# Kernel tuning notes

Hardware: AMD Instinct MI355X
Metric: run time of the kernel (lower is better)

## Reference

```python
import jax, jax.numpy as jnp
import numpy as np

B, N, D, E, H, K = 2, 2048, 1024, 8, 2048, 2


def setup_inputs() -> dict:
    key = jax.random.key(0)
    ks = jax.random.split(key, 5)
    s = 0.02  # init scale
    return {
        "x": jax.random.normal(ks[0], (B, N, D), dtype=jnp.float32),
        "w_gate": jax.random.normal(ks[1], (D, E), dtype=jnp.float32) * s,
        "b_gate": jnp.zeros((E,), dtype=jnp.float32),
        "w1": jax.random.normal(ks[2], (E, D, H), dtype=jnp.float32) * s,
        "b1": jnp.zeros((E, H), dtype=jnp.float32),
        "w2": jax.random.normal(ks[3], (E, H, D), dtype=jnp.float32) * s,
        "b2": jnp.zeros((E, D), dtype=jnp.float32),
    }


def reference(x, w_gate, b_gate, w1, b1, w2, b2):
    b, n, d = x.shape
    T = b * n
    xf = x.reshape(T, d)                                   # (T, D)
    # --- top-k routing ---
    logits = xf @ w_gate + b_gate                          # (T, E)
    topk_logits, topk_idx = jax.lax.top_k(logits, K)       # (T, K)
    topk_gates = jax.nn.softmax(topk_logits, axis=-1)      # softmax over selected experts
    entropy = -(topk_gates * jnp.log(jnp.clip(topk_gates, 1e-8, None))).sum(-1).mean()
    # scatter top-k gates into full (T, E) gate matrix (zeros for unselected)
    gates = jnp.zeros_like(logits).at[jnp.arange(T)[:, None], topk_idx].add(topk_gates)
    # --- expert MLPs (dense over experts; gates zero out unselected) ---
    h = jax.nn.relu(jnp.einsum('td,edh->eth', xf, w1) + b1[:, None, :])  # (E, T, H)
    y = jnp.einsum('eth,ehd->etd', h, w2) + b2[:, None, :]               # (E, T, D)
    out = jnp.einsum('etd,te->td', y, gates).reshape(b, n, d)
    return out, entropy
```

## Files before the change

kernel.cpp:

```cpp
#include <hip/hip_runtime.h>

#define T_TOK 4096
#define D_DIM 1024
#define E_EXP 8
#define H_DIM 2048
#define CAP   9216
#define TILES_M 72

typedef __attribute__((ext_vector_type(8))) short bf16x8;
typedef __attribute__((ext_vector_type(4))) float f32x4;

__device__ inline unsigned short f2bf(float f) {
    unsigned int u = __float_as_uint(f);
    unsigned int r = (u + 0x7fffu + ((u >> 16) & 1u)) >> 16;
    return (unsigned short)r;
}

#define GLD_LDS16(g, l)                                                        \
    __builtin_amdgcn_global_load_lds(                                          \
        (const __attribute__((address_space(1))) void*)(g),                    \
        (__attribute__((address_space(3))) void*)(l), 16, 0, 0)

__global__ void cvt_kernel(const float* __restrict__ src,
                           unsigned short* __restrict__ dst, int n4) {
    int i = blockIdx.x * blockDim.x + threadIdx.x;
    int stride = gridDim.x * blockDim.x;
    for (; i < n4; i += stride) {
        float4 v = ((const float4*)src)[i];
        ushort4 o;
        o.x = f2bf(v.x); o.y = f2bf(v.y); o.z = f2bf(v.z); o.w = f2bf(v.w);
        ((ushort4*)dst)[i] = o;
    }
}

__global__ __launch_bounds__(256) void tcvt_kernel(const float* __restrict__ src,
                                                   unsigned short* __restrict__ dst,
                                                   int R, int C) {
    __shared__ float tile[64][65];
    size_t eo = (size_t)blockIdx.z * R * C;
    src += eo; dst += eo;
    int tx = threadIdx.x & 15, ty = threadIdx.x >> 4;
    int c0 = blockIdx.x * 64, r0 = blockIdx.y * 64;
    #pragma unroll
    for (int i = 0; i < 4; i++) {
        int row = ty + i * 16;
        float4 v = *(const float4*)&src[(size_t)(r0 + row) * C + c0 + tx * 4];
        tile[row][tx * 4 + 0] = v.x;
        tile[row][tx * 4 + 1] = v.y;
        tile[row][tx * 4 + 2] = v.z;
        tile[row][tx * 4 + 3] = v.w;
    }
    __syncthreads();
    #pragma unroll
    for (int i = 0; i < 4; i++) {
        int cc = ty + i * 16;
        int rr = tx * 4;
        ushort4 o;
        o.x = f2bf(tile[rr + 0][cc]);
        o.y = f2bf(tile[rr + 1][cc]);
        o.z = f2bf(tile[rr + 2][cc]);
        o.w = f2bf(tile[rr + 3][cc]);
        *(ushort4*)&dst[(size_t)(c0 + cc) * R + r0 + rr] = o;
    }
}

__global__ __launch_bounds__(256) void gating_kernel(
    const float* __restrict__ xf, const float* __restrict__ wg,
    const float* __restrict__ bg, int* __restrict__ tk_e,
    float* __restrict__ tk_g, float* __restrict__ ent_part)
{
    __shared__ float ents[4];
    int wave = threadIdx.x >> 6, lane = threadIdx.x & 63;
    int t = blockIdx.x * 4 + wave;
    const float* xr = xf + (size_t)t * D_DIM;
    float acc[8] = {0.f,0.f,0.f,0.f,0.f,0.f,0.f,0.f};
    for (int i = 0; i < 16; i++) {
        int d = lane + i * 64;
        float xv = xr[d];
        const float4* wr = (const float4*)(wg + (size_t)d * 8);
        float4 w0 = wr[0], w1 = wr[1];
        acc[0] += xv * w0.x; acc[1] += xv * w0.y; acc[2] += xv * w0.z; acc[3] += xv * w0.w;
        acc[4] += xv * w1.x; acc[5] += xv * w1.y; acc[6] += xv * w1.z; acc[7] += xv * w1.w;
    }
    #pragma unroll
    for (int s = 1; s < 64; s <<= 1) {
        #pragma unroll
        for (int e = 0; e < 8; e++) acc[e] += __shfl_xor(acc[e], s, 64);
    }
    if (lane == 0) {
        float l[8];
        #pragma unroll
        for (int e = 0; e < 8; e++) l[e] = acc[e] + bg[e];
        int i0 = 0;
        #pragma unroll
        for (int e = 1; e < 8; e++) if (l[e] > l[i0]) i0 = e;
        int i1 = (i0 == 0) ? 1 : 0;
        #pragma unroll
        for (int e = 0; e < 8; e++) if (e != i0 && l[e] > l[i1]) i1 = e;
        float z  = expf(l[i1] - l[i0]);
        float p0 = 1.0f / (1.0f + z);
        float p1 = z / (1.0f + z);
        float ent = -(p0 * logf(fmaxf(p0, 1e-8f)) + p1 * logf(fmaxf(p1, 1e-8f)));
        ents[wave] = ent;
        tk_e[t * 2 + 0] = i0; tk_g[t * 2 + 0] = p0;
        tk_e[t * 2 + 1] = i1; tk_g[t * 2 + 1] = p1;
    }
    __syncthreads();
    if (threadIdx.x == 0)
        ent_part[blockIdx.x] = ents[0] + ents[1] + ents[2] + ents[3];
}

__global__ __launch_bounds__(256) void ent_reduce_kernel(
    const float* __restrict__ ent_part, float* __restrict__ ent_out)
{
    __shared__ float ws_[4];
    int tid = threadIdx.x;
    float s = 0.f;
    for (int i = tid; i < T_TOK / 4; i += 256) s += ent_part[i];
    #pragma unroll
    for (int d = 1; d < 64; d <<= 1) s += __shfl_xor(s, d, 64);
    if ((tid & 63) == 0) ws_[tid >> 6] = s;
    __syncthreads();
    if (tid == 0)
        *ent_out = (ws_[0] + ws_[1] + ws_[2] + ws_[3]) * (1.0f / T_TOK);
}

__global__ __launch_bounds__(1024) void route_kernel(
    const int* __restrict__ tk_e, const float* __restrict__ tk_g,
    int* __restrict__ off, int* __restrict__ slot_token,
    float* __restrict__ slot_gate, int* __restrict__ slot_of)
{
    __shared__ int wt[16][8];
    __shared__ int wx[16][8];
    __shared__ int base[9];
    __shared__ int tot[8];

    int tid = threadIdx.x, wid = tid >> 6, lane = tid & 63;
    int i0 = tid * 8;
    int ev[8];
    *(int4*)&ev[0] = *(const int4*)&tk_e[i0];
    *(int4*)&ev[4] = *(const int4*)&tk_e[i0 + 4];

    unsigned own[4] = {0u, 0u, 0u, 0u};
    #pragma unroll
    for (int j = 0; j < 8; j++) {
        int e = ev[j];
        int reg = ((e < 4) ? 0 : 2) + (e & 1);
        own[reg] += 1u << (((e >> 1) & 1) * 16);
    }
    unsigned inc[4] = {own[0], own[1], own[2], own[3]};
    #pragma unroll
    for (int d = 1; d < 64; d <<= 1) {
        #pragma unroll
        for (int k = 0; k < 4; k++) {
            unsigned t = __shfl_up(inc[k], d, 64);
            if (lane >= d) inc[k] += t;
        }
    }
    if (lane == 63) {
        #pragma unroll
        for (int e = 0; e < 8; e++) {
            int reg = ((e < 4) ? 0 : 2) + (e & 1);
            wt[wid][e] = (inc[reg] >> (((e >> 1) & 1) * 16)) & 0xFFFF;
        }
    }
    __syncthreads();
    if (tid == 0) {
        int o = 0;
        for (int e = 0; e < 8; e++) {
            int run = 0;
            for (int w = 0; w < 16; w++) { wx[w][e] = run; run += wt[w][e]; }
            tot[e] = run;
            base[e] = o;
            off[e] = o;
            o += (run + 127) & ~127;
        }
        base[8] = o;
        off[8] = o;
    }
    __syncthreads();

    #pragma unroll
    for (int e = 0; e < 8; e++) {
        int p0 = base[e] + tot[e], p1 = base[e + 1];
        for (int i = p0 + tid; i < p1; i += 1024) slot_token[i] = -1;
    }

    unsigned run[4] = {0u, 0u, 0u, 0u};
    #pragma unroll
    for (int j = 0; j < 8; j++) {
        int e = ev[j];
        int reg = ((e < 4) ? 0 : 2) + (e & 1);
        int sh = ((e >> 1) & 1) * 16;
        int lx = (int)(((inc[reg] - own[reg]) >> sh) & 0xFFFF);
        int lr = (int)((run[reg] >> sh) & 0xFFFF);
        int slot = base[e] + wx[wid][e] + lx + lr;
        run[reg] += 1u << sh;
        int i = i0 + j;
        slot_token[slot] = i >> 1;
        slot_gate[slot] = tk_g[i];
        slot_of[i] = slot;
    }
}

__global__ __launch_bounds__(256) void gemm1_kernel(
    const unsigned short* __restrict__ xb, const unsigned short* __restrict__ w1t,
    const float* __restrict__ b1g, const int* __restrict__ off,
    const int* __restrict__ slot_token, unsigned short* __restrict__ Hb)
{
    __shared__ __align__(16) unsigned short As[128 * 32];
    __shared__ __align__(16) unsigned short Bs[128 * 32];

    int s0 = blockIdx.x * 128;
    if (s0 >= off[E_EXP]) return;
    int e = 0;
    while (s0 >= off[e + 1]) e++;
    int n0 = blockIdx.y * 128;

    int tid = threadIdx.x;
    int wave = tid >> 6, lane = tid & 63;
    int lrow = lane & 15, quad = lane >> 4;
    int srow = lane >> 2;
    int scol = (lane & 3) * 8;

    int r0 = 32 * wave + srow, r1 = r0 + 16;
    int t0 = slot_token[s0 + r0]; if (t0 < 0) t0 = 0;
    int t1 = slot_token[s0 + r1]; if (t1 < 0) t1 = 0;
    const unsigned short* a0 = xb + (size_t)t0 * D_DIM + scol;
    const unsigned short* a1 = xb + (size_t)t1 * D_DIM + scol;
    const unsigned short* wb = w1t + (size_t)e * H_DIM * D_DIM;
    const unsigned short* bp0 = wb + (size_t)(n0 + r0) * D_DIM + scol;
    const unsigned short* bp1 = wb + (size_t)(n0 + r1) * D_DIM + scol;

    unsigned short* lA0 = As + wave * 1024;
    unsigned short* lA1 = lA0 + 512;
    unsigned short* lB0 = Bs + wave * 1024;
    unsigned short* lB1 = lB0 + 512;

    f32x4 acc[4][4];
    #pragma unroll
    for (int mi = 0; mi < 4; mi++)
        #pragma unroll
        for (int ni = 0; ni < 4; ni++) acc[mi][ni] = (f32x4){0.f, 0.f, 0.f, 0.f};

    int wr = (wave >> 1) * 64, wc = (wave & 1) * 64;

    for (int k0 = 0; k0 < D_DIM; k0 += 32) {
        __syncthreads();
        GLD_LDS16(a0 + k0, lA0);
        GLD_LDS16(a1 + k0, lA1);
        GLD_LDS16(bp0 + k0, lB0);
        GLD_LDS16(bp1 + k0, lB1);
        __syncthreads();
        bf16x8 af[4], bfr[4];
        #pragma unroll
        for (int i = 0; i < 4; i++) {
            af[i]  = *(const bf16x8*)&As[(wr + i * 16 + lrow) * 32 + quad * 8];
            bfr[i] = *(const bf16x8*)&Bs[(wc + i * 16 + lrow) * 32 + quad * 8];
        }
        #pragma unroll
        for (int mi = 0; mi < 4; mi++)
            #pragma unroll
            for (int ni = 0; ni < 4; ni++)
                acc[mi][ni] = __builtin_amdgcn_mfma_f32_16x16x32_bf16(
                    af[mi], bfr[ni], acc[mi][ni], 0, 0, 0);
    }

    #pragma unroll
    for (int ni = 0; ni < 4; ni++) {
        int col = wc + ni * 16 + lrow;
        int h = n0 + col;
        float bv = b1g[e * H_DIM + h];
        #pragma unroll
        for (int mi = 0; mi < 4; mi++) {
            int mrow = wr + mi * 16 + quad * 4;
            #pragma unroll
            for (int r = 0; r < 4; r++) {
                float v = fmaxf(acc[mi][ni][r] + bv, 0.0f);
                Hb[(size_t)(s0 + mrow + r) * H_DIM + h] = f2bf(v);
            }
        }
    }
}

__global__ __launch_bounds__(256) void gemm2_kernel(
    const unsigned short* __restrict__ Hb, const unsigned short* __restrict__ w2t,
    const float* __restrict__ b2g, const int* __restrict__ off,
    unsigned short* __restrict__ Yb)
{
    __shared__ __align__(16) unsigned short As[128 * 32];
    __shared__ __align__(16) unsigned short Bs[128 * 32];

    int s0 = blockIdx.x * 128;
    if (s0 >= off[E_EXP]) return;
    int e = 0;
    while (s0 >= off[e + 1]) e++;
    int n0 = blockIdx.y * 128;

    int tid = threadIdx.x;
    int wave = tid >> 6, lane = tid & 63;
    int lrow = lane & 15, quad = lane >> 4;
    int srow = lane >> 2;
    int scol = (lane & 3) * 8;

    int r0 = 32 * wave + srow, r1 = r0 + 16;
    const unsigned short* a0 = Hb + (size_t)(s0 + r0) * H_DIM + scol;
    const unsigned short* a1 = Hb + (size_t)(s0 + r1) * H_DIM + scol;
    const unsigned short* wb = w2t + (size_t)e * D_DIM * H_DIM;
    const unsigned short* bp0 = wb + (size_t)(n0 + r0) * H_DIM + scol;
    const unsigned short* bp1 = wb + (size_t)(n0 + r1) * H_DIM + scol;

    unsigned short* lA0 = As + wave * 1024;
    unsigned short* lA1 = lA0 + 512;
    unsigned short* lB0 = Bs + wave * 1024;
    unsigned short* lB1 = lB0 + 512;

    f32x4 acc[4][4];
    #pragma unroll
    for (int mi = 0; mi < 4; mi++)
        #pragma unroll
        for (int ni = 0; ni < 4; ni++) acc[mi][ni] = (f32x4){0.f, 0.f, 0.f, 0.f};

    int wr = (wave >> 1) * 64, wc = (wave & 1) * 64;

    for (int k0 = 0; k0 < H_DIM; k0 += 32) {
        __syncthreads();
        GLD_LDS16(a0 + k0, lA0);
        GLD_LDS16(a1 + k0, lA1);
        GLD_LDS16(bp0 + k0, lB0);
        GLD_LDS16(bp1 + k0, lB1);
        __syncthreads();
        bf16x8 af[4], bfr[4];
        #pragma unroll
        for (int i = 0; i < 4; i++) {
            af[i]  = *(const bf16x8*)&As[(wr + i * 16 + lrow) * 32 + quad * 8];
            bfr[i] = *(const bf16x8*)&Bs[(wc + i * 16 + lrow) * 32 + quad * 8];
        }
        #pragma unroll
        for (int mi = 0; mi < 4; mi++)
            #pragma unroll
            for (int ni = 0; ni < 4; ni++)
                acc[mi][ni] = __builtin_amdgcn_mfma_f32_16x16x32_bf16(
                    af[mi], bfr[ni], acc[mi][ni], 0, 0, 0);
    }

    #pragma unroll
    for (int ni = 0; ni < 4; ni++) {
        int col = wc + ni * 16 + lrow;
        int d = n0 + col;
        float bv = b2g[e * D_DIM + d];
        #pragma unroll
        for (int mi = 0; mi < 4; mi++) {
            int mrow = wr + mi * 16 + quad * 4;
            #pragma unroll
            for (int r = 0; r < 4; r++) {
                Yb[(size_t)(s0 + mrow + r) * D_DIM + d] = f2bf(acc[mi][ni][r] + bv);
            }
        }
    }
}

__global__ __launch_bounds__(256) void combine_kernel(
    const unsigned short* __restrict__ Yb, const int* __restrict__ slot_of,
    const float* __restrict__ tk_g, float* __restrict__ out)
{
    int t = blockIdx.x * 2 + (threadIdx.x >> 7);
    int j = threadIdx.x & 127;
    int sA = slot_of[t * 2], sB = slot_of[t * 2 + 1];
    float gA = tk_g[t * 2], gB = tk_g[t * 2 + 1];
    uint4 va = *(const uint4*)(Yb + (size_t)sA * D_DIM + j * 8);
    uint4 vb = *(const uint4*)(Yb + (size_t)sB * D_DIM + j * 8);
    const unsigned int* pa = (const unsigned int*)&va;
    const unsigned int* pb = (const unsigned int*)&vb;
    float o[8];
    #pragma unroll
    for (int i = 0; i < 4; i++) {
        float a_lo = __uint_as_float(pa[i] << 16);
        float a_hi = __uint_as_float(pa[i] & 0xffff0000u);
        float b_lo = __uint_as_float(pb[i] << 16);
        float b_hi = __uint_as_float(pb[i] & 0xffff0000u);
        o[i * 2 + 0] = gA * a_lo + gB * b_lo;
        o[i * 2 + 1] = gA * a_hi + gB * b_hi;
    }
    float* op = out + (size_t)t * D_DIM + j * 8;
    ((float4*)op)[0] = make_float4(o[0], o[1], o[2], o[3]);
    ((float4*)op)[1] = make_float4(o[4], o[5], o[6], o[7]);
}

extern "C" void kernel_launch(void* const* d_in, const int* in_sizes, int n_in,
                              void* d_out, int out_size, void* d_ws, size_t ws_size,
                              hipStream_t stream)
{
    const float* xf = (const float*)d_in[0];
    const float* wg = (const float*)d_in[1];
    const float* bg = (const float*)d_in[2];
    const float* w1 = (const float*)d_in[3];
    const float* b1 = (const float*)d_in[4];
    const float* w2 = (const float*)d_in[5];
    const float* b2 = (const float*)d_in[6];
    float* out = (float*)d_out;

    char* p = (char*)d_ws;
    int* off    = (int*)p;
    int* tk_e   = off + 16;
    float* tk_g = (float*)(tk_e + T_TOK * 2);
    int* slot_token = (int*)(tk_g + T_TOK * 2);
    float* slot_gate = (float*)(slot_token + CAP);
    int* slot_of = (int*)(slot_gate + CAP);
    float* ent_part = (float*)(slot_of + T_TOK * 2);
    size_t ofs = ((size_t)((char*)(ent_part + T_TOK / 4) - p) + 255) & ~(size_t)255;
    unsigned short* xb  = (unsigned short*)(p + ofs); ofs += (size_t)T_TOK * D_DIM * 2;
    unsigned short* w1t = (unsigned short*)(p + ofs); ofs += (size_t)E_EXP * D_DIM * H_DIM * 2;
    unsigned short* w2t = (unsigned short*)(p + ofs); ofs += (size_t)E_EXP * H_DIM * D_DIM * 2;
    unsigned short* Hb  = (unsigned short*)(p + ofs); ofs += (size_t)CAP * H_DIM * 2;
    unsigned short* Yb  = w1t;

    cvt_kernel<<<1024, 256, 0, stream>>>(xf, xb, T_TOK * D_DIM / 4);
    tcvt_kernel<<<dim3(H_DIM / 64, D_DIM / 64, E_EXP), 256, 0, stream>>>(w1, w1t, D_DIM, H_DIM);
    tcvt_kernel<<<dim3(D_DIM / 64, H_DIM / 64, E_EXP), 256, 0, stream>>>(w2, w2t, H_DIM, D_DIM);

    gating_kernel<<<T_TOK / 4, 256, 0, stream>>>(xf, wg, bg, tk_e, tk_g, ent_part);
    ent_reduce_kernel<<<1, 256, 0, stream>>>(ent_part, out + (size_t)T_TOK * D_DIM);
    route_kernel<<<1, 1024, 0, stream>>>(tk_e, tk_g, off, slot_token, slot_gate, slot_of);
    gemm1_kernel<<<dim3(TILES_M, H_DIM / 128), 256, 0, stream>>>(xb, w1t, b1, off,
                                                                 slot_token, Hb);
    gemm2_kernel<<<dim3(TILES_M, D_DIM / 128), 256, 0, stream>>>(Hb, w2t, b2, off, Yb);
    combine_kernel<<<T_TOK / 2, 256, 0, stream>>>(Yb, slot_of, tk_g, out);
}
```

Baseline: 341.0 us.

## Fuse x conversion into gating, merge entropy reduce, swizzle LDS, vectorize GEMM stores

```diff
diff --git a/kernel.cpp b/kernel.cpp
--- a/kernel.cpp
+++ b/kernel.cpp
@@ -20,18 +20,6 @@
     __builtin_amdgcn_global_load_lds(                                          \
         (const __attribute__((address_space(1))) void*)(g),                    \
         (__attribute__((address_space(3))) void*)(l), 16, 0, 0)
-
-__global__ void cvt_kernel(const float* __restrict__ src,
-                           unsigned short* __restrict__ dst, int n4) {
-    int i = blockIdx.x * blockDim.x + threadIdx.x;
-    int stride = gridDim.x * blockDim.x;
-    for (; i < n4; i += stride) {
-        float4 v = ((const float4*)src)[i];
-        ushort4 o;
-        o.x = f2bf(v.x); o.y = f2bf(v.y); o.z = f2bf(v.z); o.w = f2bf(v.w);
-        ((ushort4*)dst)[i] = o;
-    }
-}
 
 __global__ __launch_bounds__(256) void tcvt_kernel(const float* __restrict__ src,
                                                    unsigned short* __restrict__ dst,
@@ -66,17 +54,20 @@
 
 __global__ __launch_bounds__(256) void gating_kernel(
     const float* __restrict__ xf, const float* __restrict__ wg,
-    const float* __restrict__ bg, int* __restrict__ tk_e,
-    float* __restrict__ tk_g, float* __restrict__ ent_part)
+    const float* __restrict__ bg, unsigned short* __restrict__ xb,
+    int* __restrict__ tk_e, float* __restrict__ tk_g,
+    float* __restrict__ ent_part)
 {
     __shared__ float ents[4];
     int wave = threadIdx.x >> 6, lane = threadIdx.x & 63;
     int t = blockIdx.x * 4 + wave;
     const float* xr = xf + (size_t)t * D_DIM;
+    unsigned short* xbr = xb + (size_t)t * D_DIM;
     float acc[8] = {0.f,0.f,0.f,0.f,0.f,0.f,0.f,0.f};
     for (int i = 0; i < 16; i++) {
         int d = lane + i * 64;
         float xv = xr[d];
+        xbr[d] = f2bf(xv);
         const float4* wr = (const float4*)(wg + (size_t)d * 8);
         float4 w0 = wr[0], w1 = wr[1];
         acc[0] += xv * w0.x; acc[1] += xv * w0.y; acc[2] += xv * w0.z; acc[3] += xv * w0.w;
@@ -110,36 +101,28 @@
         ent_part[blockIdx.x] = ents[0] + ents[1] + ents[2] + ents[3];
 }
 
-__global__ __launch_bounds__(256) void ent_reduce_kernel(
-    const float* __restrict__ ent_part, float* __restrict__ ent_out)
-{
-    __shared__ float ws_[4];
-    int tid = threadIdx.x;
-    float s = 0.f;
-    for (int i = tid; i < T_TOK / 4; i += 256) s += ent_part[i];
-    #pragma unroll
-    for (int d = 1; d < 64; d <<= 1) s += __shfl_xor(s, d, 64);
-    if ((tid & 63) == 0) ws_[tid >> 6] = s;
-    __syncthreads();
-    if (tid == 0)
-        *ent_out = (ws_[0] + ws_[1] + ws_[2] + ws_[3]) * (1.0f / T_TOK);
-}
-
 __global__ __launch_bounds__(1024) void route_kernel(
     const int* __restrict__ tk_e, const float* __restrict__ tk_g,
     int* __restrict__ off, int* __restrict__ slot_token,
-    float* __restrict__ slot_gate, int* __restrict__ slot_of)
+    float* __restrict__ slot_gate, int* __restrict__ slot_of,
+    const float* __restrict__ ent_part, float* __restrict__ ent_out)
 {
     __shared__ int wt[16][8];
     __shared__ int wx[16][8];
     __shared__ int base[9];
     __shared__ int tot[8];
+    __shared__ float es[16];
 
     int tid = threadIdx.x, wid = tid >> 6, lane = tid & 63;
     int i0 = tid * 8;
     int ev[8];
     *(int4*)&ev[0] = *(const int4*)&tk_e[i0];
     *(int4*)&ev[4] = *(const int4*)&tk_e[i0 + 4];
+
+    float s = ent_part[tid];
+    #pragma unroll
+    for (int d = 1; d < 64; d <<= 1) s += __shfl_xor(s, d, 64);
+    if (lane == 0) es[wid] = s;
 
     unsigned own[4] = {0u, 0u, 0u, 0u};
     #pragma unroll
@@ -177,6 +160,9 @@
         }
         base[8] = o;
         off[8] = o;
+        float se = 0.f;
+        for (int w = 0; w < 16; w++) se += es[w];
+        *ent_out = se * (1.0f / T_TOK);
     }
     __syncthreads();
 
@@ -221,21 +207,21 @@
     int wave = tid >> 6, lane = tid & 63;
     int lrow = lane & 15, quad = lane >> 4;
     int srow = lane >> 2;
-    int scol = (lane & 3) * 8;
-
-    int r0 = 32 * wave + srow, r1 = r0 + 16;
+    int scol = ((lane & 3) ^ ((srow >> 1) & 3)) * 8;
+
+    int r0 = 16 * wave + srow, r1 = r0 + 64;
     int t0 = slot_token[s0 + r0]; if (t0 < 0) t0 = 0;
     int t1 = slot_token[s0 + r1]; if (t1 < 0) t1 = 0;
+    const unsigned short* wb = w1t + (size_t)e * H_DIM * D_DIM;
     const unsigned short* a0 = xb + (size_t)t0 * D_DIM + scol;
     const unsigned short* a1 = xb + (size_t)t1 * D_DIM + scol;
-    const unsigned short* wb = w1t + (size_t)e * H_DIM * D_DIM;
     const unsigned short* bp0 = wb + (size_t)(n0 + r0) * D_DIM + scol;
     const unsigned short* bp1 = wb + (size_t)(n0 + r1) * D_DIM + scol;
 
-    unsigned short* lA0 = As + wave * 1024;
-    unsigned short* lA1 = lA0 + 512;
-    unsigned short* lB0 = Bs + wave * 1024;
-    unsigned short* lB1 = lB0 + 512;
+    unsigned short* lA0 = As + (16 * wave) * 32;
+    unsigned short* lA1 = As + (64 + 16 * wave) * 32;
+    unsigned short* lB0 = Bs + (16 * wave) * 32;
+    unsigned short* lB1 = Bs + (64 + 16 * wave) * 32;
 
     f32x4 acc[4][4];
     #pragma unroll
@@ -244,6 +230,7 @@
         for (int ni = 0; ni < 4; ni++) acc[mi][ni] = (f32x4){0.f, 0.f, 0.f, 0.f};
 
     int wr = (wave >> 1) * 64, wc = (wave & 1) * 64;
+    int g = (quad ^ ((lrow >> 1) & 3)) * 8;
 
     for (int k0 = 0; k0 < D_DIM; k0 += 32) {
         __syncthreads();
@@ -255,8 +242,8 @@
         bf16x8 af[4], bfr[4];
         #pragma unroll
         for (int i = 0; i < 4; i++) {
-            af[i]  = *(const bf16x8*)&As[(wr + i * 16 + lrow) * 32 + quad * 8];
-            bfr[i] = *(const bf16x8*)&Bs[(wc + i * 16 + lrow) * 32 + quad * 8];
+            af[i]  = *(const bf16x8*)&As[(wr + i * 16 + lrow) * 32 + g];
+            bfr[i] = *(const bf16x8*)&Bs[(wc + i * 16 + lrow) * 32 + g];
         }
         #pragma unroll
         for (int mi = 0; mi < 4; mi++)
@@ -266,20 +253,25 @@
                     af[mi], bfr[ni], acc[mi][ni], 0, 0, 0);
     }
 
-    #pragma unroll
-    for (int ni = 0; ni < 4; ni++) {
-        int col = wc + ni * 16 + lrow;
-        int h = n0 + col;
-        float bv = b1g[e * H_DIM + h];
-        #pragma unroll
-        for (int mi = 0; mi < 4; mi++) {
-            int mrow = wr + mi * 16 + quad * 4;
+    float bv[4];
+    #pragma unroll
+    for (int ni = 0; ni < 4; ni++) bv[ni] = b1g[e * H_DIM + n0 + wc + ni * 16 + lrow];
+    unsigned short* w = As + wave * 1024;
+    __syncthreads();
+    #pragma unroll
+    for (int mi = 0; mi < 4; mi++) {
+        #pragma unroll
+        for (int ni = 0; ni < 4; ni++)
             #pragma unroll
-            for (int r = 0; r < 4; r++) {
-                float v = fmaxf(acc[mi][ni][r] + bv, 0.0f);
-                Hb[(size_t)(s0 + mrow + r) * H_DIM + h] = f2bf(v);
-            }
-        }
+            for (int r = 0; r < 4; r++)
+                w[(quad * 4 + r) * 64 + ni * 16 + lrow] =
+                    f2bf(fmaxf(acc[mi][ni][r] + bv[ni], 0.0f));
+        int rd = lane >> 3, cc = (lane & 7) * 8;
+        bf16x8 v0 = *(const bf16x8*)&w[rd * 64 + cc];
+        bf16x8 v1 = *(const bf16x8*)&w[(8 + rd) * 64 + cc];
+        size_t rowg = (size_t)(s0 + wr + mi * 16 + rd) * H_DIM + n0 + wc + cc;
+        *(bf16x8*)&Hb[rowg] = v0;
+        *(bf16x8*)&Hb[rowg + 8 * H_DIM] = v1;
     }
 }
 
@@ -301,19 +293,19 @@
     int wave = tid >> 6, lane = tid & 63;
     int lrow = lane & 15, quad = lane >> 4;
     int srow = lane >> 2;
-    int scol = (lane & 3) * 8;
-
-    int r0 = 32 * wave + srow, r1 = r0 + 16;
+    int scol = ((lane & 3) ^ ((srow >> 1) & 3)) * 8;
+
+    int r0 = 16 * wave + srow, r1 = r0 + 64;
+    const unsigned short* wb = w2t + (size_t)e * D_DIM * H_DIM;
     const unsigned short* a0 = Hb + (size_t)(s0 + r0) * H_DIM + scol;
     const unsigned short* a1 = Hb + (size_t)(s0 + r1) * H_DIM + scol;
-    const unsigned short* wb = w2t + (size_t)e * D_DIM * H_DIM;
     const unsigned short* bp0 = wb + (size_t)(n0 + r0) * H_DIM + scol;
     const unsigned short* bp1 = wb + (size_t)(n0 + r1) * H_DIM + scol;
 
-    unsigned short* lA0 = As + wave * 1024;
-    unsigned short* lA1 = lA0 + 512;
-    unsigned short* lB0 = Bs + wave * 1024;
-    unsigned short* lB1 = lB0 + 512;
+    unsigned short* lA0 = As + (16 * wave) * 32;
+    unsigned short* lA1 = As + (64 + 16 * wave) * 32;
+    unsigned short* lB0 = Bs + (16 * wave) * 32;
+    unsigned short* lB1 = Bs + (64 + 16 * wave) * 32;
 
     f32x4 acc[4][4];
     #pragma unroll
@@ -322,6 +314,7 @@
         for (int ni = 0; ni < 4; ni++) acc[mi][ni] = (f32x4){0.f, 0.f, 0.f, 0.f};
 
     int wr = (wave >> 1) * 64, wc = (wave & 1) * 64;
+    int g = (quad ^ ((lrow >> 1) & 3)) * 8;
 
     for (int k0 = 0; k0 < H_DIM; k0 += 32) {
         __syncthreads();
@@ -333,8 +326,8 @@
         bf16x8 af[4], bfr[4];
         #pragma unroll
         for (int i = 0; i < 4; i++) {
-            af[i]  = *(const bf16x8*)&As[(wr + i * 16 + lrow) * 32 + quad * 8];
-            bfr[i] = *(const bf16x8*)&Bs[(wc + i * 16 + lrow) * 32 + quad * 8];
+            af[i]  = *(const bf16x8*)&As[(wr + i * 16 + lrow) * 32 + g];
+            bfr[i] = *(const bf16x8*)&Bs[(wc + i * 16 + lrow) * 32 + g];
         }
         #pragma unroll
         for (int mi = 0; mi < 4; mi++)
@@ -344,19 +337,24 @@
                     af[mi], bfr[ni], acc[mi][ni], 0, 0, 0);
     }
 
-    #pragma unroll
-    for (int ni = 0; ni < 4; ni++) {
-        int col = wc + ni * 16 + lrow;
-        int d = n0 + col;
-        float bv = b2g[e * D_DIM + d];
-        #pragma unroll
-        for (int mi = 0; mi < 4; mi++) {
-            int mrow = wr + mi * 16 + quad * 4;
+    float bv[4];
+    #pragma unroll
+    for (int ni = 0; ni < 4; ni++) bv[ni] = b2g[e * D_DIM + n0 + wc + ni * 16 + lrow];
+    unsigned short* w = As + wave * 1024;
+    __syncthreads();
+    #pragma unroll
+    for (int mi = 0; mi < 4; mi++) {
+        #pragma unroll
+        for (int ni = 0; ni < 4; ni++)
             #pragma unroll
-            for (int r = 0; r < 4; r++) {
-                Yb[(size_t)(s0 + mrow + r) * D_DIM + d] = f2bf(acc[mi][ni][r] + bv);
-            }
-        }
+            for (int r = 0; r < 4; r++)
+                w[(quad * 4 + r) * 64 + ni * 16 + lrow] = f2bf(acc[mi][ni][r] + bv[ni]);
+        int rd = lane >> 3, cc = (lane & 7) * 8;
+        bf16x8 v0 = *(const bf16x8*)&w[rd * 64 + cc];
+        bf16x8 v1 = *(const bf16x8*)&w[(8 + rd) * 64 + cc];
+        size_t rowg = (size_t)(s0 + wr + mi * 16 + rd) * D_DIM + n0 + wc + cc;
+        *(bf16x8*)&Yb[rowg] = v0;
+        *(bf16x8*)&Yb[rowg + 8 * D_DIM] = v1;
     }
 }
 
@@ -415,13 +413,11 @@
     unsigned short* Hb  = (unsigned short*)(p + ofs); ofs += (size_t)CAP * H_DIM * 2;
     unsigned short* Yb  = w1t;
 
-    cvt_kernel<<<1024, 256, 0, stream>>>(xf, xb, T_TOK * D_DIM / 4);
+    gating_kernel<<<T_TOK / 4, 256, 0, stream>>>(xf, wg, bg, xb, tk_e, tk_g, ent_part);
+    route_kernel<<<1, 1024, 0, stream>>>(tk_e, tk_g, off, slot_token, slot_gate, slot_of,
+                                         ent_part, out + (size_t)T_TOK * D_DIM);
     tcvt_kernel<<<dim3(H_DIM / 64, D_DIM / 64, E_EXP), 256, 0, stream>>>(w1, w1t, D_DIM, H_DIM);
     tcvt_kernel<<<dim3(D_DIM / 64, H_DIM / 64, E_EXP), 256, 0, stream>>>(w2, w2t, H_DIM, D_DIM);
-
-    gating_kernel<<<T_TOK / 4, 256, 0, stream>>>(xf, wg, bg, tk_e, tk_g, ent_part);
-    ent_reduce_kernel<<<1, 256, 0, stream>>>(ent_part, out + (size_t)T_TOK * D_DIM);
-    route_kernel<<<1, 1024, 0, stream>>>(tk_e, tk_g, off, slot_token, slot_gate, slot_of);
     gemm1_kernel<<<dim3(TILES_M, H_DIM / 128), 256, 0, stream>>>(xb, w1t, b1, off,
                                                                  slot_token, Hb);
     gemm2_kernel<<<dim3(TILES_M, D_DIM / 128), 256, 0, stream>>>(Hb, w2t, b2, off, Yb);
```

Measured after the change: 329.5 us. -3.4%, faster.
